# Kernel tuning notes

Measured on AMD Instinct MI355X. Metric: run time of the kernel, lower is better.

The kernel has to match this reference:

```python
import jax, jax.numpy as jnp
import numpy as np

N = 4096
D_MODEL = 512


def setup_inputs() -> dict:
    key = jax.random.key(0)
    ks = jax.random.split(key, 5)
    scale = 1.0 / np.sqrt(D_MODEL)
    return {
        "x": jax.random.normal(ks[0], (N, D_MODEL), dtype=jnp.float32),
        "Wq": jax.random.normal(ks[1], (D_MODEL, D_MODEL), dtype=jnp.float32) * scale,
        "Wk": jax.random.normal(ks[2], (D_MODEL, D_MODEL), dtype=jnp.float32) * scale,
        "Wv": jax.random.normal(ks[3], (D_MODEL, D_MODEL), dtype=jnp.float32) * scale,
        "Ws": jax.random.normal(ks[4], (1, D_MODEL), dtype=jnp.float32) * scale,
    }


def reference(x, Wq, Wk, Wv, Ws):
    # x: [N, d]; torch nn.Linear(bias=False) computes x @ W.T
    Q = x @ Wq.T  # [N, d]
    K = x @ Wk.T  # [N, d]
    V = x @ Wv.T  # [N, d]
    sigma = jnp.clip(x @ Ws.T, 0.001, 1.0)  # [N, 1]

    # prior association: Gaussian kernel over |i - j| with per-row sigma
    pos = jnp.arange(sigma.shape[0], dtype=jnp.float32)
    diff = jnp.abs(pos[:, None] - pos[None, :])  # [N, N]
    gaussian = jnp.exp(-0.5 * (diff / sigma) ** 2) / jnp.sqrt(2.0 * jnp.pi * sigma)
    P = gaussian / (gaussian.sum(axis=1, keepdims=True) + 1e-8)

    scale = jnp.sqrt(jnp.float32(x.shape[-1]))
    S = jax.nn.softmax((Q @ K.T) / scale, axis=-1)  # [N, N]
    Z = S @ V  # [N, d]
    return Z, P, S
```

## Files before the change

kernel.cpp:

```cpp
#include <hip/hip_runtime.h>
#include <math.h>

#define N_TOK 4096
#define DM 512

typedef _Float16 f16x8 __attribute__((ext_vector_type(8)));
typedef _Float16 f16x4 __attribute__((ext_vector_type(4)));
typedef float f32x4 __attribute__((ext_vector_type(4)));

__device__ __forceinline__ void async_ld16(const ushort* g, ushort* l) {
  __builtin_amdgcn_global_load_lds(
      (const __attribute__((address_space(1))) void*)g,
      (__attribute__((address_space(3))) void*)l, 16, 0, 0);
}

__global__ __launch_bounds__(256) void pack16(const float* __restrict__ src,
                                              _Float16* __restrict__ dst) {
  int i = (blockIdx.x * 256 + threadIdx.x) * 4;
  float4 v = *(const float4*)&src[i];
  f16x4 o;
  o.x = (_Float16)v.x; o.y = (_Float16)v.y;
  o.z = (_Float16)v.z; o.w = (_Float16)v.w;
  *(f16x4*)&dst[i] = o;
}

template <int EPI>
__global__ __launch_bounds__(256) void mfma_f16(
    const _Float16* __restrict__ A, int lda, const _Float16* __restrict__ B,
    int ldb, int K, float scale, float* __restrict__ Cf, int ldc,
    _Float16* __restrict__ Q16, _Float16* __restrict__ K16,
    float* __restrict__ Vf, float* __restrict__ PartA,
    float* __restrict__ PartB) {
  __shared__ _Float16 lds[2 * 128 * 32];
  _Float16* Ah = lds;
  _Float16* Bh = lds + 128 * 32;

  const int t = threadIdx.x;
  const int w = t >> 6, L = t & 63;
  const int wm = (w >> 1) * 64, wn = (w & 1) * 64;
  const int row = L & 15, quad = L >> 4;
  const int bm = blockIdx.y * 128, bn = blockIdx.x * 128;
  const int kbase = blockIdx.z * K;

  f32x4 acc[4][4] = {{}};

  const int c0 = t, c1 = t + 256;
  const int r0 = c0 >> 2, o0 = (c0 & 3) * 8;
  const int r1 = r0 + 64;

  const ushort* ga0 = (const ushort*)(A + (size_t)(bm + r0) * lda + kbase + o0);
  const ushort* ga1 = (const ushort*)(A + (size_t)(bm + r1) * lda + kbase + o0);
  const ushort* gb0 = (const ushort*)(B + (size_t)(bn + r0) * ldb + kbase + o0);
  const ushort* gb1 = (const ushort*)(B + (size_t)(bn + r1) * ldb + kbase + o0);

  for (int k0 = 0; k0 < K; k0 += 32) {
    async_ld16(ga0, (ushort*)(Ah + c0 * 8));
    async_ld16(ga1, (ushort*)(Ah + c1 * 8));
    async_ld16(gb0, (ushort*)(Bh + c0 * 8));
    async_ld16(gb1, (ushort*)(Bh + c1 * 8));
    ga0 += 32; ga1 += 32; gb0 += 32; gb1 += 32;
    __syncthreads();

    f16x8 a0[4], b0[4];
#pragma unroll
    for (int i = 0; i < 4; ++i)
      a0[i] = *(const f16x8*)&Ah[(wm + i * 16 + row) * 32 + quad * 8];
#pragma unroll
    for (int j = 0; j < 4; ++j)
      b0[j] = *(const f16x8*)&Bh[(wn + j * 16 + row) * 32 + quad * 8];
#pragma unroll
    for (int i = 0; i < 4; ++i)
#pragma unroll
      for (int j = 0; j < 4; ++j)
        acc[i][j] = __builtin_amdgcn_mfma_f32_16x16x32_f16(a0[i], b0[j],
                                                           acc[i][j], 0, 0, 0);
    __syncthreads();
  }

  if (EPI == 0) {
#pragma unroll
    for (int i = 0; i < 4; ++i)
#pragma unroll
      for (int j = 0; j < 4; ++j)
#pragma unroll
        for (int r = 0; r < 4; ++r) {
          int gr = bm + wm + i * 16 + quad * 4 + r;
          int gc = bn + wn + j * 16 + row;
          Cf[(size_t)gr * ldc + gc] = acc[i][j][r] * scale;
        }
  } else if (EPI == 1) {
    const int region = bn >> 9;
#pragma unroll
    for (int i = 0; i < 4; ++i)
#pragma unroll
      for (int j = 0; j < 4; ++j)
#pragma unroll
        for (int r = 0; r < 4; ++r) {
          int gr = bm + wm + i * 16 + quad * 4 + r;
          int nn = (bn & 511) + wn + j * 16 + row;
          float v = acc[i][j][r];
          if (region == 2) {
            Vf[(size_t)gr * 512 + nn] = v;
          } else {
            _Float16* D = region ? K16 : Q16;
            D[(size_t)gr * 512 + nn] = (_Float16)v;
          }
        }
  } else {
    const int z = blockIdx.z;
    float* dst = (z == 0) ? Cf
                          : ((z < 3) ? PartA + (size_t)(z - 1) * 2097152
                                     : PartB);
#pragma unroll
    for (int i = 0; i < 4; ++i)
#pragma unroll
      for (int j = 0; j < 4; ++j)
#pragma unroll
        for (int r = 0; r < 4; ++r) {
          int gr = bm + wm + i * 16 + quad * 4 + r;
          int gc = bn + wn + j * 16 + row;
          dst[(size_t)gr * ldc + gc] = acc[i][j][r] * scale;
        }
  }
}

__global__ __launch_bounds__(256) void reduce_z(float* __restrict__ Z,
                                                const float* __restrict__ PartA,
                                                const float* __restrict__ PartB) {
  int i = (blockIdx.x * 256 + threadIdx.x) * 4;
  float4 z = *(const float4*)&Z[i];
  float4 a = *(const float4*)&PartA[i];
  float4 b = *(const float4*)&PartA[2097152 + i];
  float4 c = *(const float4*)&PartB[i];
  z.x += a.x + b.x + c.x;
  z.y += a.y + b.y + c.y;
  z.z += a.z + b.z + c.z;
  z.w += a.w + b.w + c.w;
  *(float4*)&Z[i] = z;
}

__global__ __launch_bounds__(256) void transpose_v(const float* __restrict__ Vf,
                                                   _Float16* __restrict__ VT) {
  __shared__ float T[32][33];
  const int t = threadIdx.x;
  const int r = t >> 3, c4 = (t & 7) * 4;
  float4 v = *(const float4*)&Vf[(size_t)(blockIdx.y * 32 + r) * 512 +
                                 blockIdx.x * 32 + c4];
  T[r][c4] = v.x; T[r][c4 + 1] = v.y; T[r][c4 + 2] = v.z; T[r][c4 + 3] = v.w;
  __syncthreads();
  f16x4 o;
  o.x = (_Float16)T[c4][r];
  o.y = (_Float16)T[c4 + 1][r];
  o.z = (_Float16)T[c4 + 2][r];
  o.w = (_Float16)T[c4 + 3][r];
  *(f16x4*)&VT[(size_t)(blockIdx.x * 32 + r) * 4096 + blockIdx.y * 32 + c4] = o;
}

__global__ __launch_bounds__(256) void sigma_kernel(const float* __restrict__ x,
                                                    const float* __restrict__ Ws,
                                                    float* __restrict__ sigma) {
  const int wave = threadIdx.x >> 6;
  const int lane = threadIdx.x & 63;
  const int row = blockIdx.x * 4 + wave;
  const float4* xr = (const float4*)(x + (size_t)row * DM);
  const float4* w = (const float4*)Ws;
  float s = 0.f;
#pragma unroll
  for (int r = 0; r < 2; ++r) {
    float4 a = xr[lane + 64 * r];
    float4 b = w[lane + 64 * r];
    s += a.x * b.x + a.y * b.y + a.z * b.z + a.w * b.w;
  }
#pragma unroll
  for (int off = 32; off > 0; off >>= 1) s += __shfl_down(s, off);
  if (lane == 0) sigma[row] = fminf(fmaxf(s, 0.001f), 1.0f);
}

__global__ __launch_bounds__(256) void softmax_kernel(float* __restrict__ S,
                                                      _Float16* __restrict__ S16) {
  __shared__ float red[256];
  const int t = threadIdx.x;
  float* Srow = S + (size_t)blockIdx.x * N_TOK;
  _Float16* S16row = S16 + (size_t)blockIdx.x * N_TOK;
  float4 v[4];
  float m = -INFINITY;
#pragma unroll
  for (int r = 0; r < 4; ++r) {
    v[r] = *(float4*)&Srow[r * 1024 + t * 4];
    m = fmaxf(m, fmaxf(fmaxf(v[r].x, v[r].y), fmaxf(v[r].z, v[r].w)));
  }
  red[t] = m;
  __syncthreads();
  for (int off = 128; off > 0; off >>= 1) {
    if (t < off) red[t] = fmaxf(red[t], red[t + off]);
    __syncthreads();
  }
  m = red[0];
  __syncthreads();
  float sum = 0.f;
#pragma unroll
  for (int r = 0; r < 4; ++r) {
    v[r].x = __expf(v[r].x - m);
    v[r].y = __expf(v[r].y - m);
    v[r].z = __expf(v[r].z - m);
    v[r].w = __expf(v[r].w - m);
    sum += v[r].x + v[r].y + v[r].z + v[r].w;
  }
  red[t] = sum;
  __syncthreads();
  for (int off = 128; off > 0; off >>= 1) {
    if (t < off) red[t] += red[t + off];
    __syncthreads();
  }
  const float inv = 1.0f / red[0];
#pragma unroll
  for (int r = 0; r < 4; ++r) {
    v[r].x *= inv; v[r].y *= inv; v[r].z *= inv; v[r].w *= inv;
    *(float4*)&Srow[r * 1024 + t * 4] = v[r];
    f16x4 o;
    o.x = (_Float16)v[r].x; o.y = (_Float16)v[r].y;
    o.z = (_Float16)v[r].z; o.w = (_Float16)v[r].w;
    *(f16x4*)&S16row[r * 1024 + t * 4] = o;
  }
}

__global__ __launch_bounds__(256) void p_kernel(const float* __restrict__ sigma,
                                                float* __restrict__ P) {
  __shared__ float red[256];
  const int i = blockIdx.x;
  const int t = threadIdx.x;
  const float sg = sigma[i];
  const float inv2 = -0.5f / (sg * sg);
  const float c = rsqrtf(6.283185307179586f * sg);
  float4 g[4];
  float sum = 0.f;
#pragma unroll
  for (int r = 0; r < 4; ++r) {
    int j = r * 1024 + t * 4;
    float d0 = (float)(i - j);
    float d1 = (float)(i - j - 1);
    float d2 = (float)(i - j - 2);
    float d3 = (float)(i - j - 3);
    g[r].x = __expf(inv2 * d0 * d0) * c;
    g[r].y = __expf(inv2 * d1 * d1) * c;
    g[r].z = __expf(inv2 * d2 * d2) * c;
    g[r].w = __expf(inv2 * d3 * d3) * c;
    sum += g[r].x + g[r].y + g[r].z + g[r].w;
  }
  red[t] = sum;
  __syncthreads();
  for (int off = 128; off > 0; off >>= 1) {
    if (t < off) red[t] += red[t + off];
    __syncthreads();
  }
  const float inv = 1.0f / (red[0] + 1e-8f);
  float* Prow = P + (size_t)i * N_TOK;
#pragma unroll
  for (int r = 0; r < 4; ++r) {
    g[r].x *= inv; g[r].y *= inv; g[r].z *= inv; g[r].w *= inv;
    *(float4*)&Prow[r * 1024 + t * 4] = g[r];
  }
}

extern "C" void kernel_launch(void* const* d_in, const int* in_sizes, int n_in,
                              void* d_out, int out_size, void* d_ws,
                              size_t ws_size, hipStream_t stream) {
  const float* x = (const float*)d_in[0];
  const float* Wq = (const float*)d_in[1];
  const float* Wk = (const float*)d_in[2];
  const float* Wv = (const float*)d_in[3];
  const float* Ws = (const float*)d_in[4];

  float* out = (float*)d_out;
  float* Z = out;
  float* Pout = Z + (size_t)N_TOK * DM;
  float* S = Pout + (size_t)N_TOK * N_TOK;

  const size_t E = (size_t)N_TOK * DM;
  _Float16* Q16 = (_Float16*)Pout;
  _Float16* K16 = Q16 + E;
  float* Vf = (float*)(K16 + E);
  _Float16* VT16 = (_Float16*)(Vf + E);
  _Float16* S16 = VT16 + E;
  float* PartA = (float*)Pout;
  float* PartB = (float*)(S16 + (size_t)N_TOK * N_TOK);

  _Float16* x16 = (_Float16*)d_ws;
  _Float16* Wc16 = x16 + E;
  float* sg = (float*)(Wc16 + 3 * DM * DM);

  const dim3 blk(256);

  pack16<<<E / 1024, blk, 0, stream>>>(x, x16);
  pack16<<<DM * DM / 1024, blk, 0, stream>>>(Wq, Wc16);
  pack16<<<DM * DM / 1024, blk, 0, stream>>>(Wk, Wc16 + DM * DM);
  pack16<<<DM * DM / 1024, blk, 0, stream>>>(Wv, Wc16 + 2 * DM * DM);
  sigma_kernel<<<N_TOK / 4, blk, 0, stream>>>(x, Ws, sg);

  mfma_f16<1><<<dim3(12, 32), blk, 0, stream>>>(
      x16, DM, Wc16, DM, DM, 1.0f, nullptr, 0, Q16, K16, Vf, nullptr, nullptr);

  transpose_v<<<dim3(16, 128), blk, 0, stream>>>(Vf, VT16);

  mfma_f16<0><<<dim3(32, 32), blk, 0, stream>>>(
      Q16, DM, K16, DM, DM, 1.0f / sqrtf((float)DM), S, N_TOK, nullptr,
      nullptr, nullptr, nullptr, nullptr);

  softmax_kernel<<<N_TOK, blk, 0, stream>>>(S, S16);

  mfma_f16<2><<<dim3(4, 32, 4), blk, 0, stream>>>(
      S16, N_TOK, VT16, N_TOK, N_TOK / 4, 1.0f, Z, DM, nullptr, nullptr,
      nullptr, PartA, PartB);
  reduce_z<<<E / 1024, blk, 0, stream>>>(Z, PartA, PartB);

  p_kernel<<<N_TOK, blk, 0, stream>>>(sg, Pout);
}
```

Baseline: 280.3 us.

## Store score and V intermediates in fp16 and fuse small kernels

The QK^T GEMM now writes the scaled scores as fp16 rather than fp32. Softmax reads those fp16 values and writes both the fp32 S output and an in-place fp16 copy. This cuts global-memory traffic on the largest N×N intermediate. V is also produced directly in fp16, so the transpose only moves half-width data. The three weight-pack kernels, the x pack and the sigma reduction are merged into one launch, and the Z partial-sum reduction is folded into the P kernel launch. The Z partials move into the workspace. In exchange, scores are rounded to fp16 before softmax, which loses some precision, and the workspace must be large enough to hold the partials.

```diff
diff --git a/kernel.cpp b/kernel.cpp
--- a/kernel.cpp
+++ b/kernel.cpp
@@ -14,23 +14,56 @@
       (__attribute__((address_space(3))) void*)l, 16, 0, 0);
 }
 
-__global__ __launch_bounds__(256) void pack16(const float* __restrict__ src,
-                                              _Float16* __restrict__ dst) {
-  int i = (blockIdx.x * 256 + threadIdx.x) * 4;
-  float4 v = *(const float4*)&src[i];
-  f16x4 o;
-  o.x = (_Float16)v.x; o.y = (_Float16)v.y;
-  o.z = (_Float16)v.z; o.w = (_Float16)v.w;
-  *(f16x4*)&dst[i] = o;
+__global__ __launch_bounds__(256) void pack_sigma(
+    const float* __restrict__ x, const float* __restrict__ Wq,
+    const float* __restrict__ Wk, const float* __restrict__ Wv,
+    const float* __restrict__ Ws, _Float16* __restrict__ x16,
+    _Float16* __restrict__ Wc16, float* __restrict__ sg) {
+  const int b = blockIdx.x;
+  const int t = threadIdx.x;
+  if (b < 2048) {
+    int i = b * 1024 + t * 4;
+    float4 v = *(const float4*)&x[i];
+    f16x4 o;
+    o.x = (_Float16)v.x; o.y = (_Float16)v.y;
+    o.z = (_Float16)v.z; o.w = (_Float16)v.w;
+    *(f16x4*)&x16[i] = o;
+    int col = (t * 4) & 511;
+    float4 w = *(const float4*)&Ws[col];
+    float p = v.x * w.x + v.y * w.y + v.z * w.z + v.w * w.w;
+    __shared__ float red[256];
+    red[t] = p;
+    __syncthreads();
+    int lt = t & 127;
+    for (int off = 64; off > 0; off >>= 1) {
+      if (lt < off) red[t] += red[t + off];
+      __syncthreads();
+    }
+    if (lt == 0) {
+      float s = red[t];
+      sg[2 * b + (t >> 7)] = fminf(fmaxf(s, 0.001f), 1.0f);
+    }
+  } else {
+    int e = (b - 2048) * 1024 + t * 4;
+    const float* src;
+    int le = e & (DM * DM - 1);
+    if (e < DM * DM) src = Wq + le;
+    else if (e < 2 * DM * DM) src = Wk + le;
+    else src = Wv + le;
+    float4 v = *(const float4*)src;
+    f16x4 o;
+    o.x = (_Float16)v.x; o.y = (_Float16)v.y;
+    o.z = (_Float16)v.z; o.w = (_Float16)v.w;
+    *(f16x4*)&Wc16[e] = o;
+  }
 }
 
 template <int EPI>
 __global__ __launch_bounds__(256) void mfma_f16(
     const _Float16* __restrict__ A, int lda, const _Float16* __restrict__ B,
     int ldb, int K, float scale, float* __restrict__ Cf, int ldc,
-    _Float16* __restrict__ Q16, _Float16* __restrict__ K16,
-    float* __restrict__ Vf, float* __restrict__ PartA,
-    float* __restrict__ PartB) {
+    _Float16* __restrict__ D0, _Float16* __restrict__ D1,
+    _Float16* __restrict__ D2, float* __restrict__ Part) {
   __shared__ _Float16 lds[2 * 128 * 32];
   _Float16* Ah = lds;
   _Float16* Bh = lds + 128 * 32;
@@ -77,7 +110,20 @@
     __syncthreads();
   }
 
-  if (EPI == 0) {
+  if (EPI == 1) {
+    const int region = bn >> 9;
+    _Float16* D = (region == 0) ? D0 : ((region == 1) ? D1 : D2);
+#pragma unroll
+    for (int i = 0; i < 4; ++i)
+#pragma unroll
+      for (int j = 0; j < 4; ++j)
+#pragma unroll
+        for (int r = 0; r < 4; ++r) {
+          int gr = bm + wm + i * 16 + quad * 4 + r;
+          int nn = (bn & 511) + wn + j * 16 + row;
+          D[(size_t)gr * 512 + nn] = (_Float16)acc[i][j][r];
+        }
+  } else if (EPI == 3) {
 #pragma unroll
     for (int i = 0; i < 4; ++i)
 #pragma unroll
@@ -86,31 +132,11 @@
         for (int r = 0; r < 4; ++r) {
           int gr = bm + wm + i * 16 + quad * 4 + r;
           int gc = bn + wn + j * 16 + row;
-          Cf[(size_t)gr * ldc + gc] = acc[i][j][r] * scale;
-        }
-  } else if (EPI == 1) {
-    const int region = bn >> 9;
-#pragma unroll
-    for (int i = 0; i < 4; ++i)
-#pragma unroll
-      for (int j = 0; j < 4; ++j)
-#pragma unroll
-        for (int r = 0; r < 4; ++r) {
-          int gr = bm + wm + i * 16 + quad * 4 + r;
-          int nn = (bn & 511) + wn + j * 16 + row;
-          float v = acc[i][j][r];
-          if (region == 2) {
-            Vf[(size_t)gr * 512 + nn] = v;
-          } else {
-            _Float16* D = region ? K16 : Q16;
-            D[(size_t)gr * 512 + nn] = (_Float16)v;
-          }
+          D0[(size_t)gr * ldc + gc] = (_Float16)(acc[i][j][r] * scale);
         }
   } else {
     const int z = blockIdx.z;
-    float* dst = (z == 0) ? Cf
-                          : ((z < 3) ? PartA + (size_t)(z - 1) * 2097152
-                                     : PartB);
+    float* dst = (z == 0) ? Cf : (Part + (size_t)(z - 1) * 2097152);
 #pragma unroll
     for (int i = 0; i < 4; ++i)
 #pragma unroll
@@ -124,70 +150,35 @@
   }
 }
 
-__global__ __launch_bounds__(256) void reduce_z(float* __restrict__ Z,
-                                                const float* __restrict__ PartA,
-                                                const float* __restrict__ PartB) {
-  int i = (blockIdx.x * 256 + threadIdx.x) * 4;
-  float4 z = *(const float4*)&Z[i];
-  float4 a = *(const float4*)&PartA[i];
-  float4 b = *(const float4*)&PartA[2097152 + i];
-  float4 c = *(const float4*)&PartB[i];
-  z.x += a.x + b.x + c.x;
-  z.y += a.y + b.y + c.y;
-  z.z += a.z + b.z + c.z;
-  z.w += a.w + b.w + c.w;
-  *(float4*)&Z[i] = z;
-}
-
-__global__ __launch_bounds__(256) void transpose_v(const float* __restrict__ Vf,
-                                                   _Float16* __restrict__ VT) {
-  __shared__ float T[32][33];
+__global__ __launch_bounds__(256) void transpose16(
+    const _Float16* __restrict__ V16, _Float16* __restrict__ VT) {
+  __shared__ _Float16 T[32][34];
   const int t = threadIdx.x;
   const int r = t >> 3, c4 = (t & 7) * 4;
-  float4 v = *(const float4*)&Vf[(size_t)(blockIdx.y * 32 + r) * 512 +
-                                 blockIdx.x * 32 + c4];
+  f16x4 v = *(const f16x4*)&V16[(size_t)(blockIdx.y * 32 + r) * 512 +
+                                blockIdx.x * 32 + c4];
   T[r][c4] = v.x; T[r][c4 + 1] = v.y; T[r][c4 + 2] = v.z; T[r][c4 + 3] = v.w;
   __syncthreads();
   f16x4 o;
-  o.x = (_Float16)T[c4][r];
-  o.y = (_Float16)T[c4 + 1][r];
-  o.z = (_Float16)T[c4 + 2][r];
-  o.w = (_Float16)T[c4 + 3][r];
+  o.x = T[c4][r]; o.y = T[c4 + 1][r]; o.z = T[c4 + 2][r]; o.w = T[c4 + 3][r];
   *(f16x4*)&VT[(size_t)(blockIdx.x * 32 + r) * 4096 + blockIdx.y * 32 + c4] = o;
 }
 
-__global__ __launch_bounds__(256) void sigma_kernel(const float* __restrict__ x,
-                                                    const float* __restrict__ Ws,
-                                                    float* __restrict__ sigma) {
-  const int wave = threadIdx.x >> 6;
-  const int lane = threadIdx.x & 63;
-  const int row = blockIdx.x * 4 + wave;
-  const float4* xr = (const float4*)(x + (size_t)row * DM);
-  const float4* w = (const float4*)Ws;
-  float s = 0.f;
-#pragma unroll
-  for (int r = 0; r < 2; ++r) {
-    float4 a = xr[lane + 64 * r];
-    float4 b = w[lane + 64 * r];
-    s += a.x * b.x + a.y * b.y + a.z * b.z + a.w * b.w;
-  }
-#pragma unroll
-  for (int off = 32; off > 0; off >>= 1) s += __shfl_down(s, off);
-  if (lane == 0) sigma[row] = fminf(fmaxf(s, 0.001f), 1.0f);
-}
-
-__global__ __launch_bounds__(256) void softmax_kernel(float* __restrict__ S,
-                                                      _Float16* __restrict__ S16) {
+__global__ __launch_bounds__(256) void softmax_kernel(
+    _Float16* __restrict__ Sc, float* __restrict__ S) {
   __shared__ float red[256];
   const int t = threadIdx.x;
+  _Float16* Srow16 = Sc + (size_t)blockIdx.x * N_TOK;
   float* Srow = S + (size_t)blockIdx.x * N_TOK;
-  _Float16* S16row = S16 + (size_t)blockIdx.x * N_TOK;
-  float4 v[4];
+  float f[16];
   float m = -INFINITY;
 #pragma unroll
   for (int r = 0; r < 4; ++r) {
-    v[r] = *(float4*)&Srow[r * 1024 + t * 4];
-    m = fmaxf(m, fmaxf(fmaxf(v[r].x, v[r].y), fmaxf(v[r].z, v[r].w)));
+    f16x4 h = *(const f16x4*)&Srow16[r * 1024 + t * 4];
+    f[r * 4 + 0] = (float)h.x; f[r * 4 + 1] = (float)h.y;
+    f[r * 4 + 2] = (float)h.z; f[r * 4 + 3] = (float)h.w;
+    m = fmaxf(m, fmaxf(fmaxf(f[r * 4], f[r * 4 + 1]),
+                       fmaxf(f[r * 4 + 2], f[r * 4 + 3])));
   }
   red[t] = m;
   __syncthreads();
@@ -199,12 +190,9 @@
   __syncthreads();
   float sum = 0.f;
 #pragma unroll
-  for (int r = 0; r < 4; ++r) {
-    v[r].x = __expf(v[r].x - m);
-    v[r].y = __expf(v[r].y - m);
-    v[r].z = __expf(v[r].z - m);
-    v[r].w = __expf(v[r].w - m);
-    sum += v[r].x + v[r].y + v[r].z + v[r].w;
+  for (int i = 0; i < 16; ++i) {
+    f[i] = __expf(f[i] - m);
+    sum += f[i];
   }
   red[t] = sum;
   __syncthreads();
@@ -215,20 +203,36 @@
   const float inv = 1.0f / red[0];
 #pragma unroll
   for (int r = 0; r < 4; ++r) {
-    v[r].x *= inv; v[r].y *= inv; v[r].z *= inv; v[r].w *= inv;
-    *(float4*)&Srow[r * 1024 + t * 4] = v[r];
-    f16x4 o;
-    o.x = (_Float16)v[r].x; o.y = (_Float16)v[r].y;
-    o.z = (_Float16)v[r].z; o.w = (_Float16)v[r].w;
-    *(f16x4*)&S16row[r * 1024 + t * 4] = o;
-  }
-}
-
-__global__ __launch_bounds__(256) void p_kernel(const float* __restrict__ sigma,
-                                                float* __restrict__ P) {
+    float4 o;
+    o.x = f[r * 4 + 0] * inv; o.y = f[r * 4 + 1] * inv;
+    o.z = f[r * 4 + 2] * inv; o.w = f[r * 4 + 3] * inv;
+    *(float4*)&Srow[r * 1024 + t * 4] = o;
+    f16x4 h;
+    h.x = (_Float16)o.x; h.y = (_Float16)o.y;
+    h.z = (_Float16)o.z; h.w = (_Float16)o.w;
+    *(f16x4*)&Srow16[r * 1024 + t * 4] = h;
+  }
+}
+
+__global__ __launch_bounds__(256) void tail_kernel(
+    const float* __restrict__ sigma, float* __restrict__ P,
+    float* __restrict__ Z, const float* __restrict__ Part) {
+  const int t = threadIdx.x;
+  if (blockIdx.x >= 4096) {
+    int i = (blockIdx.x - 4096) * 1024 + t * 4;
+    float4 z = *(const float4*)&Z[i];
+    float4 a = *(const float4*)&Part[i];
+    float4 b = *(const float4*)&Part[2097152 + i];
+    float4 c = *(const float4*)&Part[2 * 2097152 + i];
+    z.x += a.x + b.x + c.x;
+    z.y += a.y + b.y + c.y;
+    z.z += a.z + b.z + c.z;
+    z.w += a.w + b.w + c.w;
+    *(float4*)&Z[i] = z;
+    return;
+  }
   __shared__ float red[256];
   const int i = blockIdx.x;
-  const int t = threadIdx.x;
   const float sg = sigma[i];
   const float inv2 = -0.5f / (sg * sg);
   const float c = rsqrtf(6.283185307179586f * sg);
@@ -279,39 +283,33 @@
   const size_t E = (size_t)N_TOK * DM;
   _Float16* Q16 = (_Float16*)Pout;
   _Float16* K16 = Q16 + E;
-  float* Vf = (float*)(K16 + E);
-  _Float16* VT16 = (_Float16*)(Vf + E);
-  _Float16* S16 = VT16 + E;
-  float* PartA = (float*)Pout;
-  float* PartB = (float*)(S16 + (size_t)N_TOK * N_TOK);
+  _Float16* V16 = K16 + E;
+  _Float16* VT16 = V16 + E;
+  _Float16* Sc16 = VT16 + E;
 
   _Float16* x16 = (_Float16*)d_ws;
   _Float16* Wc16 = x16 + E;
   float* sg = (float*)(Wc16 + 3 * DM * DM);
+  float* Part = sg + 4096;
 
   const dim3 blk(256);
 
-  pack16<<<E / 1024, blk, 0, stream>>>(x, x16);
-  pack16<<<DM * DM / 1024, blk, 0, stream>>>(Wq, Wc16);
-  pack16<<<DM * DM / 1024, blk, 0, stream>>>(Wk, Wc16 + DM * DM);
-  pack16<<<DM * DM / 1024, blk, 0, stream>>>(Wv, Wc16 + 2 * DM * DM);
-  sigma_kernel<<<N_TOK / 4, blk, 0, stream>>>(x, Ws, sg);
+  pack_sigma<<<2816, blk, 0, stream>>>(x, Wq, Wk, Wv, Ws, x16, Wc16, sg);
 
   mfma_f16<1><<<dim3(12, 32), blk, 0, stream>>>(
-      x16, DM, Wc16, DM, DM, 1.0f, nullptr, 0, Q16, K16, Vf, nullptr, nullptr);
-
-  transpose_v<<<dim3(16, 128), blk, 0, stream>>>(Vf, VT16);
-
-  mfma_f16<0><<<dim3(32, 32), blk, 0, stream>>>(
-      Q16, DM, K16, DM, DM, 1.0f / sqrtf((float)DM), S, N_TOK, nullptr,
-      nullptr, nullptr, nullptr, nullptr);
-
-  softmax_kernel<<<N_TOK, blk, 0, stream>>>(S, S16);
+      x16, DM, Wc16, DM, DM, 1.0f, nullptr, 0, Q16, K16, V16, nullptr);
+
+  transpose16<<<dim3(16, 128), blk, 0, stream>>>(V16, VT16);
+
+  mfma_f16<3><<<dim3(32, 32), blk, 0, stream>>>(
+      Q16, DM, K16, DM, DM, 1.0f / sqrtf((float)DM), nullptr, N_TOK, Sc16,
+      nullptr, nullptr, nullptr);
+
+  softmax_kernel<<<N_TOK, blk, 0, stream>>>(Sc16, S);
 
   mfma_f16<2><<<dim3(4, 32, 4), blk, 0, stream>>>(
-      S16, N_TOK, VT16, N_TOK, N_TOK / 4, 1.0f, Z, DM, nullptr, nullptr,
-      nullptr, PartA, PartB);
-  reduce_z<<<E / 1024, blk, 0, stream>>>(Z, PartA, PartB);
-
-  p_kernel<<<N_TOK, blk, 0, stream>>>(sg, Pout);
-}
+      Sc16, N_TOK, VT16, N_TOK, N_TOK / 4, 1.0f, Z, DM, nullptr, nullptr,
+      nullptr, Part);
+
+  tail_kernel<<<4096 + 2048, blk, 0, stream>>>(sg, Pout, Z, Part);
+}
```

Result: faster. 262.0 us (-6.5%).
